# Kernel optimization log

Hardware: AMD Instinct MI355X
Metric: run time of the kernel (lower is better)

Reference implementation:

```python
import jax, jax.numpy as jnp
import numpy as np

B, Q, HID = 8, 8, 4096
H, KVH, D = 32, 8, 128
KV = 4096
ROPE_THETA = 10000.0


def rotate_half(x):
    x1, x2 = jnp.split(x, 2, axis=-1)
    return jnp.concatenate([-x2, x1], axis=-1)


def setup_inputs() -> dict:
    key = jax.random.key(0)
    ks = jax.random.split(key, 6)
    hidden_states = jax.random.normal(ks[0], (B, Q, HID), dtype=jnp.float32)
    position_ids = jnp.broadcast_to(jnp.arange(KV, dtype=jnp.int64), (B, KV))
    key_cache = jax.random.normal(ks[1], (B, KVH, KV, D), dtype=jnp.float32)
    value_cache = jax.random.normal(ks[2], (B, KVH, KV, D), dtype=jnp.float32)
    # mask: True -> blocked (-10000). Queries occupy last Q positions, causal.
    qpos = KV - Q + jnp.arange(Q)
    attention_mask = (jnp.arange(KV)[None, :] > qpos[:, None])[None, None]  # [1,1,Q,KV]
    attention_mask = jnp.broadcast_to(attention_mask, (B, 1, Q, KV))
    q_w = jax.random.normal(ks[3], (HID, HID), dtype=jnp.float32) * 0.02
    o_w = jax.random.normal(ks[4], (HID, HID), dtype=jnp.float32) * 0.02
    return {"hidden_states": hidden_states, "position_ids": position_ids,
            "key_cache": key_cache, "value_cache": value_cache,
            "attention_mask": attention_mask, "q_w": q_w, "o_w": o_w}


def reference(hidden_states, position_ids, key_cache, value_cache, attention_mask, q_w, o_w):
    # q projection: nn.Linear -> x @ W^T
    q = hidden_states @ q_w.T                       # [B,Q,HID]
    q = q.reshape(B, Q, H, D).transpose(0, 2, 1, 3)  # [B,H,Q,D]

    # rotary tables for kv_seq_len positions
    half = D // 2
    inv_freq = 1.0 / (ROPE_THETA ** (jnp.arange(0, half, dtype=jnp.float32) / half))
    t = jnp.arange(KV, dtype=jnp.float32)
    freqs = t[:, None] * inv_freq[None, :]           # [KV, D/2]
    emb = jnp.concatenate([freqs, freqs], axis=-1)   # [KV, D]
    cos_t, sin_t = jnp.cos(emb), jnp.sin(emb)

    # position_idx trick from the module: single effective rope position
    idx = jnp.argmax(position_ids.astype(jnp.int32), axis=1)[0]
    pid = jnp.take(position_ids, idx[None], axis=1)  # [B,1]
    cos = cos_t[pid][:, None]                        # [B,1,1,D]
    sin = sin_t[pid][:, None]
    q = q * cos + rotate_half(q) * sin               # [B,H,Q,D]

    # GQA attention without materializing repeat_kv (same math)
    G = H // KVH
    qg = q.reshape(B, KVH, G, Q, D)
    scores = jnp.einsum('bkgqd,bksd->bkgqs', qg, key_cache) / jnp.sqrt(jnp.float32(D))
    mask = attention_mask[:, :, None]                # [B,1,1,Q,KV]
    scores = jnp.where(mask, jnp.float32(-10000.0), scores)
    probs = jax.nn.softmax(scores.astype(jnp.float32), axis=-1).astype(q.dtype)
    out = jnp.einsum('bkgqs,bksd->bkgqd', probs, value_cache)  # [B,KVH,G,Q,D]
    out = out.reshape(B, H, Q, D).transpose(0, 2, 1, 3).reshape(B, Q, HID)
    return out @ o_w.T
```

## Files before the change

kernel.cpp:

```cpp
#include <hip/hip_runtime.h>
#include <math.h>

#define B_   8
#define Q_   8
#define HID  4096
#define NH   32
#define KVH_ 8
#define GQ   4
#define D_   128
#define KV_  4096
#define M_   64

#define OFF_COS   0
#define OFF_SIN   512
#define OFF_QROPE 1024
#define OFF_ATT   (OFF_QROPE + M_*HID)
#define OFF_OPART (OFF_ATT + M_*HID)
#define OFF_MPART (OFF_OPART + 64*8*32*128)
#define OFF_LPART (OFF_MPART + 64*8*32)
#define OFF_GPART (OFF_LPART + 64*8*32)

__global__ void prep_kernel(const int* __restrict__ pos, float* __restrict__ ws) {
    __shared__ int sv[256], si[256];
    __shared__ int s_idx;
    int t = threadIdx.x;
    int bv = -2147483647 - 1, bi = 0x7fffffff;
    for (int i = t; i < KV_; i += 256) {
        int v = pos[i];
        if (v > bv || (v == bv && i < bi)) { bv = v; bi = i; }
    }
    sv[t] = bv; si[t] = bi;
    __syncthreads();
    for (int off = 128; off > 0; off >>= 1) {
        if (t < off) {
            int v2 = sv[t + off], i2 = si[t + off];
            if (v2 > sv[t] || (v2 == sv[t] && i2 < si[t])) { sv[t] = v2; si[t] = i2; }
        }
        __syncthreads();
    }
    if (t == 0) s_idx = si[0];
    __syncthreads();
    int idx = s_idx;
    for (int u = t; u < B_ * 64; u += 256) {
        int b = u >> 6, d = u & 63;
        int pid = pos[b * KV_ + idx];
        float inv = __expf(-(float)d * (9.210340371976184f / 64.0f));
        float f = (float)pid * inv;
        ws[OFF_COS + u] = cosf(f);
        ws[OFF_SIN + u] = sinf(f);
    }
}

__global__ __launch_bounds__(128) void gemm_part(const float* __restrict__ A,
                                                 const float* __restrict__ W,
                                                 float* __restrict__ part) {
    __shared__ __align__(16) float As[32][68];
    __shared__ __align__(16) float Ws[32][132];
    int nc = blockIdx.x, kc = blockIdx.y;
    int t = threadIdx.x;
    int k0 = kc * 256;
    int n0 = nc * 128;
    int tx = t & 15, ty = t >> 4;
    float acc[2][2][4][4];
    #pragma unroll
    for (int a = 0; a < 2; a++)
        for (int bq = 0; bq < 2; bq++)
            for (int i = 0; i < 4; i++)
                for (int j = 0; j < 4; j++) acc[a][bq][i][j] = 0.f;

    for (int kt = 0; kt < 8; ++kt) {
        int kb = k0 + kt * 32;
        __syncthreads();
        {
            int m = t & 63, qh = t >> 6;
            #pragma unroll
            for (int c = 0; c < 4; ++c) {
                int q = qh * 4 + c;
                float4 v = *(const float4*)(A + (size_t)m * HID + kb + q * 4);
                As[q*4+0][m] = v.x; As[q*4+1][m] = v.y; As[q*4+2][m] = v.z; As[q*4+3][m] = v.w;
            }
        }
        {
            int n = t;
            const float* wr = W + (size_t)(n0 + n) * HID + kb;
            #pragma unroll
            for (int c = 0; c < 8; ++c) {
                float4 v = *(const float4*)(wr + c * 4);
                Ws[c*4+0][n] = v.x; Ws[c*4+1][n] = v.y; Ws[c*4+2][n] = v.z; Ws[c*4+3][n] = v.w;
            }
        }
        __syncthreads();
        #pragma unroll
        for (int kk = 0; kk < 32; ++kk) {
            float4 a0 = *(const float4*)&As[kk][ty * 4];
            float4 a1 = *(const float4*)&As[kk][32 + ty * 4];
            float4 w0 = *(const float4*)&Ws[kk][tx * 4];
            float4 w1 = *(const float4*)&Ws[kk][64 + tx * 4];
            float am[2][4] = {{a0.x,a0.y,a0.z,a0.w},{a1.x,a1.y,a1.z,a1.w}};
            float wn[2][4] = {{w0.x,w0.y,w0.z,w0.w},{w1.x,w1.y,w1.z,w1.w}};
            #pragma unroll
            for (int a = 0; a < 2; a++)
            #pragma unroll
            for (int bq = 0; bq < 2; bq++)
            #pragma unroll
            for (int i = 0; i < 4; i++)
            #pragma unroll
            for (int j = 0; j < 4; j++)
                acc[a][bq][i][j] += am[a][i] * wn[bq][j];
        }
    }
    #pragma unroll
    for (int a = 0; a < 2; a++) {
        #pragma unroll
        for (int i = 0; i < 4; i++) {
            int m = a * 32 + ty * 4 + i;
            float* dst = part + ((size_t)kc * 64 + m) * HID + n0;
            #pragma unroll
            for (int bq = 0; bq < 2; bq++) {
                float4 v;
                v.x = acc[a][bq][i][0]; v.y = acc[a][bq][i][1];
                v.z = acc[a][bq][i][2]; v.w = acc[a][bq][i][3];
                *(float4*)(dst + bq * 64 + tx * 4) = v;
            }
        }
    }
}

__global__ void qrope_kernel(float* ws) {
    const float* part = ws + OFF_GPART;
    int blk = blockIdx.x;
    int b = blk >> 5, h = blk & 31;
    int t = threadIdx.x;
    int qq = t >> 5, dl = t & 31;
    int m = b * 8 + qq;
    int d0 = dl * 2;
    float x0 = 0, x1 = 0, y0 = 0, y1 = 0;
    const float* pbase = part + (size_t)m * HID + h * 128;
    #pragma unroll
    for (int kc = 0; kc < 16; ++kc) {
        const float* p = pbase + (size_t)kc * 64 * HID;
        x0 += p[d0];      x1 += p[d0 + 1];
        y0 += p[d0 + 64]; y1 += p[d0 + 65];
    }
    float c0 = ws[OFF_COS + b * 64 + d0], c1 = ws[OFF_COS + b * 64 + d0 + 1];
    float s0 = ws[OFF_SIN + b * 64 + d0], s1 = ws[OFF_SIN + b * 64 + d0 + 1];
    float* qr = ws + OFF_QROPE + ((size_t)(b * 32 + h)) * Q_ * D_ + (size_t)qq * D_;
    qr[d0]      = x0 * c0 - y0 * s0;
    qr[d0 + 1]  = x1 * c1 - y1 * s1;
    qr[d0 + 64] = y0 * c0 + x0 * s0;
    qr[d0 + 65] = y1 * c1 + x1 * s1;
}

#define CHUNK 512
#define TK 64
__global__ __launch_bounds__(128) void attn_kernel(const float* __restrict__ Kc,
                                                   const float* __restrict__ Vc,
                                                   float* __restrict__ ws) {
    __shared__ __align__(16) float qT[128][36];
    __shared__ __align__(16) float kv[128 * 68];
    __shared__ __align__(16) float pT[64][36];
    __shared__ float m_st[32], l_st[32], al_st[32];

    int c = blockIdx.x, kvh = blockIdx.y, b = blockIdx.z;
    int t = threadIdx.x;
    int pair = b * 8 + kvh;
    const float* qbase = ws + OFF_QROPE + (size_t)pair * 32 * 128;
    {
        int r = t & 31, qh = t >> 5;
        #pragma unroll
        for (int cq = 0; cq < 8; ++cq) {
            int dq = qh * 8 + cq;
            float4 v = *(const float4*)(qbase + (size_t)r * 128 + dq * 4);
            qT[dq*4+0][r] = v.x; qT[dq*4+1][r] = v.y; qT[dq*4+2][r] = v.z; qT[dq*4+3][r] = v.w;
        }
    }
    if (t < 32) { m_st[t] = -INFINITY; l_st[t] = 0.f; }

    int rt = t >> 4, st = t & 15;
    int dt = t & 15;
    float o[4][8];
    #pragma unroll
    for (int i = 0; i < 4; i++)
        for (int j = 0; j < 8; j++) o[i][j] = 0.f;

    const float* Kb = Kc + ((size_t)pair * KV_ + c * CHUNK) * D_;
    const float* Vb = Vc + ((size_t)pair * KV_ + c * CHUNK) * D_;
    const float scale = 0.08838834764831845f;

    for (int T = 0; T < CHUNK / TK; ++T) {
        int s0 = T * TK;
        __syncthreads();
        {
            int s = t >> 1, half = t & 1;
            const float* kr = Kb + (size_t)(s0 + s) * D_ + half * 64;
            #pragma unroll
            for (int cq = 0; cq < 16; ++cq) {
                float4 v = *(const float4*)(kr + cq * 4);
                int d = half * 64 + cq * 4;
                kv[(d+0)*68 + s] = v.x; kv[(d+1)*68 + s] = v.y;
                kv[(d+2)*68 + s] = v.z; kv[(d+3)*68 + s] = v.w;
            }
        }
        __syncthreads();
        float S[4][4];
        #pragma unroll
        for (int i = 0; i < 4; i++)
            for (int j = 0; j < 4; j++) S[i][j] = 0.f;
        #pragma unroll 4
        for (int d = 0; d < 128; ++d) {
            float4 q4 = *(const float4*)&qT[d][rt * 4];
            float4 k4 = *(const float4*)&kv[d * 68 + st * 4];
            float qa[4] = {q4.x, q4.y, q4.z, q4.w};
            float ka[4] = {k4.x, k4.y, k4.z, k4.w};
            #pragma unroll
            for (int i = 0; i < 4; i++)
            #pragma unroll
            for (int j = 0; j < 4; j++)
                S[i][j] += qa[i] * ka[j];
        }
        int sabs_base = c * CHUNK + s0 + st * 4;
        #pragma unroll
        for (int i = 0; i < 4; i++) {
            int r = rt * 4 + i;
            int qq = r & 7;
            int qpos = KV_ - Q_ + qq;
            float v[4];
            float rmax = -INFINITY;
            #pragma unroll
            for (int j = 0; j < 4; j++) {
                int sa = sabs_base + j;
                float x = (sa > qpos) ? -10000.0f : S[i][j] * scale;
                v[j] = x;
                rmax = fmaxf(rmax, x);
            }
            for (int ml = 1; ml <= 8; ml <<= 1) rmax = fmaxf(rmax, __shfl_xor(rmax, ml, 64));
            float m_old = m_st[r];
            float m_new = fmaxf(m_old, rmax);
            float al = __expf(m_old - m_new);
            float ps = 0.f;
            #pragma unroll
            for (int j = 0; j < 4; j++) {
                float p = __expf(v[j] - m_new);
                pT[st * 4 + j][r] = p;
                ps += p;
            }
            for (int ml = 1; ml <= 8; ml <<= 1) ps += __shfl_xor(ps, ml, 64);
            if (st == 0) {
                l_st[r] = l_st[r] * al + ps;
                m_st[r] = m_new;
                al_st[r] = al;
            }
        }
        __syncthreads();
        {
            int s = t >> 1, half = t & 1;
            const float* vr = Vb + (size_t)(s0 + s) * D_ + half * 64;
            float* dst = &kv[s * 132 + half * 64];
            #pragma unroll
            for (int cq = 0; cq < 16; ++cq)
                *(float4*)(dst + cq * 4) = *(const float4*)(vr + cq * 4);
        }
        __syncthreads();
        float al4[4];
        #pragma unroll
        for (int i = 0; i < 4; i++) al4[i] = al_st[rt * 4 + i];
        #pragma unroll
        for (int i = 0; i < 4; i++)
            for (int j = 0; j < 8; j++) o[i][j] *= al4[i];
        #pragma unroll 2
        for (int s = 0; s < TK; ++s) {
            float4 p4 = *(const float4*)&pT[s][rt * 4];
            float4 v0 = *(const float4*)&kv[s * 132 + dt * 8];
            float4 v1 = *(const float4*)&kv[s * 132 + dt * 8 + 4];
            float pp[4] = {p4.x, p4.y, p4.z, p4.w};
            float vv[8] = {v0.x, v0.y, v0.z, v0.w, v1.x, v1.y, v1.z, v1.w};
            #pragma unroll
            for (int i = 0; i < 4; i++)
            #pragma unroll
            for (int j = 0; j < 8; j++)
                o[i][j] += pp[i] * vv[j];
        }
    }
    float* opart = ws + OFF_OPART + ((size_t)pair * 8 + c) * 32 * 128;
    #pragma unroll
    for (int i = 0; i < 4; i++) {
        int r = rt * 4 + i;
        float* dst = opart + (size_t)r * 128 + dt * 8;
        float4 v0, v1;
        v0.x = o[i][0]; v0.y = o[i][1]; v0.z = o[i][2]; v0.w = o[i][3];
        v1.x = o[i][4]; v1.y = o[i][5]; v1.z = o[i][6]; v1.w = o[i][7];
        *(float4*)dst = v0; *(float4*)(dst + 4) = v1;
    }
    __syncthreads();
    if (t < 32) {
        ws[OFF_MPART + ((size_t)pair * 8 + c) * 32 + t] = m_st[t];
        ws[OFF_LPART + ((size_t)pair * 8 + c) * 32 + t] = l_st[t];
    }
}

__global__ void combine_kernel(float* ws) {
    __shared__ float w_sh[8][32];
    int pair = blockIdx.x;
    int b = pair >> 3, kvh = pair & 7;
    int t = threadIdx.x;
    if (t < 32) {
        int r = t;
        float M = -INFINITY;
        float mv[8];
        #pragma unroll
        for (int cc = 0; cc < 8; ++cc) {
            mv[cc] = ws[OFF_MPART + ((size_t)pair * 8 + cc) * 32 + r];
            M = fmaxf(M, mv[cc]);
        }
        float L = 0.f;
        float e[8];
        #pragma unroll
        for (int cc = 0; cc < 8; ++cc) {
            e[cc] = __expf(mv[cc] - M);
            L += e[cc] * ws[OFF_LPART + ((size_t)pair * 8 + cc) * 32 + r];
        }
        float invL = 1.f / L;
        #pragma unroll
        for (int cc = 0; cc < 8; ++cc) w_sh[cc][r] = e[cc] * invL;
    }
    __syncthreads();
    const float* opart = ws + OFF_OPART + (size_t)pair * 8 * 32 * 128;
    float* aout = ws + OFF_ATT;
    for (int idx = t; idx < 32 * 128; idx += 256) {
        int r = idx >> 7, d = idx & 127;
        float acc = 0.f;
        #pragma unroll
        for (int cc = 0; cc < 8; ++cc)
            acc += w_sh[cc][r] * opart[((size_t)cc * 32 + r) * 128 + d];
        int g = r >> 3, qq = r & 7;
        aout[((size_t)(b * 8 + qq)) * HID + (kvh * 4 + g) * 128 + d] = acc;
    }
}

__global__ void oreduce_kernel(const float* __restrict__ part, float* __restrict__ out) {
    int idx = blockIdx.x * 256 + threadIdx.x;
    float4 acc = {0, 0, 0, 0};
    const float4* p = (const float4*)part;
    #pragma unroll
    for (int kc = 0; kc < 16; ++kc) {
        float4 v = p[(size_t)kc * 65536 + idx];
        acc.x += v.x; acc.y += v.y; acc.z += v.z; acc.w += v.w;
    }
    ((float4*)out)[idx] = acc;
}

extern "C" void kernel_launch(void* const* d_in, const int* in_sizes, int n_in,
                              void* d_out, int out_size, void* d_ws, size_t ws_size,
                              hipStream_t stream) {
    const float* hidden = (const float*)d_in[0];
    const int*   pos    = (const int*)d_in[1];
    const float* kcache = (const float*)d_in[2];
    const float* vcache = (const float*)d_in[3];
    const float* qw = (const float*)d_in[5];
    const float* ow = (const float*)d_in[6];
    float* ws  = (float*)d_ws;
    float* out = (float*)d_out;
    float* gpart = ws + OFF_GPART;

    prep_kernel<<<1, 256, 0, stream>>>(pos, ws);
    gemm_part<<<dim3(32, 16), 128, 0, stream>>>(hidden, qw, gpart);
    qrope_kernel<<<256, 256, 0, stream>>>(ws);
    attn_kernel<<<dim3(8, 8, 8), 128, 0, stream>>>(kcache, vcache, ws);
    combine_kernel<<<64, 256, 0, stream>>>(ws);
    gemm_part<<<dim3(32, 16), 128, 0, stream>>>(ws + OFF_ATT, ow, gpart);
    oreduce_kernel<<<256, 256, 0, stream>>>(gpart, out);
}
```

Before: 500.0 us.

## Double-buffer GEMM tiles, halve N tile, split attention over 256 threads

The GEMM now uses 64-wide N tiles, which doubles the grid to 1024 blocks, and double-buffers its shared-memory tiles with register prefetch of the next K slice, so there is one barrier per step. The attention kernel moves to 256 threads: QK^T is split across two D halves and combined with a lane shuffle, and the PV product reads V directly from global memory instead of staging it in shared memory, which removes a barrier pair. The aim is more parallelism, latency hiding, and less shared-memory traffic. The cost is more blocks and possibly uncoalesced or repeated global V reads.

```diff
diff --git a/kernel.cpp b/kernel.cpp
--- a/kernel.cpp
+++ b/kernel.cpp
@@ -54,75 +54,80 @@
 __global__ __launch_bounds__(128) void gemm_part(const float* __restrict__ A,
                                                  const float* __restrict__ W,
                                                  float* __restrict__ part) {
-    __shared__ __align__(16) float As[32][68];
-    __shared__ __align__(16) float Ws[32][132];
+    __shared__ __align__(16) float As[2][32][68];
+    __shared__ __align__(16) float Ws[2][32][68];
     int nc = blockIdx.x, kc = blockIdx.y;
     int t = threadIdx.x;
     int k0 = kc * 256;
-    int n0 = nc * 128;
+    int n0 = nc * 64;
     int tx = t & 15, ty = t >> 4;
-    float acc[2][2][4][4];
-    #pragma unroll
-    for (int a = 0; a < 2; a++)
-        for (int bq = 0; bq < 2; bq++)
-            for (int i = 0; i < 4; i++)
-                for (int j = 0; j < 4; j++) acc[a][bq][i][j] = 0.f;
-
+    int sr = t & 63, sq = t >> 6;
+
+    const float* arow = A + (size_t)sr * HID + k0 + sq * 16;
+    const float* wrow = W + (size_t)(n0 + sr) * HID + k0 + sq * 16;
+
+    float acc[8][4];
+    #pragma unroll
+    for (int i = 0; i < 8; i++)
+        #pragma unroll
+        for (int j = 0; j < 4; j++) acc[i][j] = 0.f;
+
+    #pragma unroll
+    for (int c = 0; c < 4; ++c) {
+        float4 av = *(const float4*)(arow + c * 4);
+        float4 wv = *(const float4*)(wrow + c * 4);
+        int q = sq * 4 + c;
+        As[0][q*4+0][sr] = av.x; As[0][q*4+1][sr] = av.y;
+        As[0][q*4+2][sr] = av.z; As[0][q*4+3][sr] = av.w;
+        Ws[0][q*4+0][sr] = wv.x; Ws[0][q*4+1][sr] = wv.y;
+        Ws[0][q*4+2][sr] = wv.z; Ws[0][q*4+3][sr] = wv.w;
+    }
+    __syncthreads();
+
+    int cur = 0;
     for (int kt = 0; kt < 8; ++kt) {
-        int kb = k0 + kt * 32;
-        __syncthreads();
-        {
-            int m = t & 63, qh = t >> 6;
+        float4 ra[4], rw[4];
+        if (kt < 7) {
             #pragma unroll
             for (int c = 0; c < 4; ++c) {
-                int q = qh * 4 + c;
-                float4 v = *(const float4*)(A + (size_t)m * HID + kb + q * 4);
-                As[q*4+0][m] = v.x; As[q*4+1][m] = v.y; As[q*4+2][m] = v.z; As[q*4+3][m] = v.w;
-            }
-        }
-        {
-            int n = t;
-            const float* wr = W + (size_t)(n0 + n) * HID + kb;
-            #pragma unroll
-            for (int c = 0; c < 8; ++c) {
-                float4 v = *(const float4*)(wr + c * 4);
-                Ws[c*4+0][n] = v.x; Ws[c*4+1][n] = v.y; Ws[c*4+2][n] = v.z; Ws[c*4+3][n] = v.w;
-            }
-        }
-        __syncthreads();
+                ra[c] = *(const float4*)(arow + (kt + 1) * 32 + c * 4);
+                rw[c] = *(const float4*)(wrow + (kt + 1) * 32 + c * 4);
+            }
+        }
         #pragma unroll
         for (int kk = 0; kk < 32; ++kk) {
-            float4 a0 = *(const float4*)&As[kk][ty * 4];
-            float4 a1 = *(const float4*)&As[kk][32 + ty * 4];
-            float4 w0 = *(const float4*)&Ws[kk][tx * 4];
-            float4 w1 = *(const float4*)&Ws[kk][64 + tx * 4];
-            float am[2][4] = {{a0.x,a0.y,a0.z,a0.w},{a1.x,a1.y,a1.z,a1.w}};
-            float wn[2][4] = {{w0.x,w0.y,w0.z,w0.w},{w1.x,w1.y,w1.z,w1.w}};
-            #pragma unroll
-            for (int a = 0; a < 2; a++)
-            #pragma unroll
-            for (int bq = 0; bq < 2; bq++)
-            #pragma unroll
-            for (int i = 0; i < 4; i++)
-            #pragma unroll
-            for (int j = 0; j < 4; j++)
-                acc[a][bq][i][j] += am[a][i] * wn[bq][j];
-        }
-    }
-    #pragma unroll
-    for (int a = 0; a < 2; a++) {
-        #pragma unroll
-        for (int i = 0; i < 4; i++) {
-            int m = a * 32 + ty * 4 + i;
-            float* dst = part + ((size_t)kc * 64 + m) * HID + n0;
-            #pragma unroll
-            for (int bq = 0; bq < 2; bq++) {
-                float4 v;
-                v.x = acc[a][bq][i][0]; v.y = acc[a][bq][i][1];
-                v.z = acc[a][bq][i][2]; v.w = acc[a][bq][i][3];
-                *(float4*)(dst + bq * 64 + tx * 4) = v;
-            }
-        }
+            float4 a0 = *(const float4*)&As[cur][kk][ty * 8];
+            float4 a1 = *(const float4*)&As[cur][kk][ty * 8 + 4];
+            float4 w0 = *(const float4*)&Ws[cur][kk][tx * 4];
+            float am[8] = {a0.x,a0.y,a0.z,a0.w,a1.x,a1.y,a1.z,a1.w};
+            float wn[4] = {w0.x,w0.y,w0.z,w0.w};
+            #pragma unroll
+            for (int i = 0; i < 8; i++)
+                #pragma unroll
+                for (int j = 0; j < 4; j++)
+                    acc[i][j] += am[i] * wn[j];
+        }
+        if (kt < 7) {
+            int nb = cur ^ 1;
+            #pragma unroll
+            for (int c = 0; c < 4; ++c) {
+                int q = sq * 4 + c;
+                As[nb][q*4+0][sr] = ra[c].x; As[nb][q*4+1][sr] = ra[c].y;
+                As[nb][q*4+2][sr] = ra[c].z; As[nb][q*4+3][sr] = ra[c].w;
+                Ws[nb][q*4+0][sr] = rw[c].x; Ws[nb][q*4+1][sr] = rw[c].y;
+                Ws[nb][q*4+2][sr] = rw[c].z; Ws[nb][q*4+3][sr] = rw[c].w;
+            }
+            __syncthreads();
+            cur = nb;
+        }
+    }
+    #pragma unroll
+    for (int i = 0; i < 8; i++) {
+        int m = ty * 8 + i;
+        float* dst = part + ((size_t)kc * 64 + m) * HID + n0 + tx * 4;
+        float4 v;
+        v.x = acc[i][0]; v.y = acc[i][1]; v.z = acc[i][2]; v.w = acc[i][3];
+        *(float4*)dst = v;
     }
 }
 
@@ -153,11 +158,11 @@
 
 #define CHUNK 512
 #define TK 64
-__global__ __launch_bounds__(128) void attn_kernel(const float* __restrict__ Kc,
+__global__ __launch_bounds__(256) void attn_kernel(const float* __restrict__ Kc,
                                                    const float* __restrict__ Vc,
                                                    float* __restrict__ ws) {
     __shared__ __align__(16) float qT[128][36];
-    __shared__ __align__(16) float kv[128 * 68];
+    __shared__ __align__(16) float kT[128][68];
     __shared__ __align__(16) float pT[64][36];
     __shared__ float m_st[32], l_st[32], al_st[32];
 
@@ -168,20 +173,25 @@
     {
         int r = t & 31, qh = t >> 5;
         #pragma unroll
-        for (int cq = 0; cq < 8; ++cq) {
-            int dq = qh * 8 + cq;
+        for (int cq = 0; cq < 4; ++cq) {
+            int dq = qh + cq * 8;
             float4 v = *(const float4*)(qbase + (size_t)r * 128 + dq * 4);
-            qT[dq*4+0][r] = v.x; qT[dq*4+1][r] = v.y; qT[dq*4+2][r] = v.z; qT[dq*4+3][r] = v.w;
+            qT[dq*4+0][r] = v.x; qT[dq*4+1][r] = v.y;
+            qT[dq*4+2][r] = v.z; qT[dq*4+3][r] = v.w;
         }
     }
     if (t < 32) { m_st[t] = -INFINITY; l_st[t] = 0.f; }
 
-    int rt = t >> 4, st = t & 15;
-    int dt = t & 15;
-    float o[4][8];
+    int st = t & 15;
+    int dh = (t >> 4) & 1;
+    int rt = t >> 5;
+    int dt = t & 31;
+
+    float o[4][4];
     #pragma unroll
     for (int i = 0; i < 4; i++)
-        for (int j = 0; j < 8; j++) o[i][j] = 0.f;
+        #pragma unroll
+        for (int j = 0; j < 4; j++) o[i][j] = 0.f;
 
     const float* Kb = Kc + ((size_t)pair * KV_ + c * CHUNK) * D_;
     const float* Vb = Vc + ((size_t)pair * KV_ + c * CHUNK) * D_;
@@ -191,25 +201,28 @@
         int s0 = T * TK;
         __syncthreads();
         {
-            int s = t >> 1, half = t & 1;
-            const float* kr = Kb + (size_t)(s0 + s) * D_ + half * 64;
-            #pragma unroll
-            for (int cq = 0; cq < 16; ++cq) {
-                float4 v = *(const float4*)(kr + cq * 4);
-                int d = half * 64 + cq * 4;
-                kv[(d+0)*68 + s] = v.x; kv[(d+1)*68 + s] = v.y;
-                kv[(d+2)*68 + s] = v.z; kv[(d+3)*68 + s] = v.w;
+            int s = t >> 2, qr = t & 3;
+            const float* kr = Kb + (size_t)(s0 + s) * D_ + qr * 4;
+            #pragma unroll
+            for (int cq = 0; cq < 8; ++cq) {
+                float4 v = *(const float4*)(kr + cq * 16);
+                int d = qr * 4 + cq * 16;
+                kT[d+0][s] = v.x; kT[d+1][s] = v.y;
+                kT[d+2][s] = v.z; kT[d+3][s] = v.w;
             }
         }
         __syncthreads();
         float S[4][4];
         #pragma unroll
         for (int i = 0; i < 4; i++)
+            #pragma unroll
             for (int j = 0; j < 4; j++) S[i][j] = 0.f;
+        int dbase = dh * 64;
         #pragma unroll 4
-        for (int d = 0; d < 128; ++d) {
+        for (int dd = 0; dd < 64; ++dd) {
+            int d = dbase + dd;
             float4 q4 = *(const float4*)&qT[d][rt * 4];
-            float4 k4 = *(const float4*)&kv[d * 68 + st * 4];
+            float4 k4 = *(const float4*)&kT[d][st * 4];
             float qa[4] = {q4.x, q4.y, q4.z, q4.w};
             float ka[4] = {k4.x, k4.y, k4.z, k4.w};
             #pragma unroll
@@ -218,6 +231,11 @@
             for (int j = 0; j < 4; j++)
                 S[i][j] += qa[i] * ka[j];
         }
+        #pragma unroll
+        for (int i = 0; i < 4; i++)
+            #pragma unroll
+            for (int j = 0; j < 4; j++)
+                S[i][j] += __shfl_xor(S[i][j], 16, 64);
         int sabs_base = c * CHUNK + s0 + st * 4;
         #pragma unroll
         for (int i = 0; i < 4; i++) {
@@ -241,43 +259,35 @@
             #pragma unroll
             for (int j = 0; j < 4; j++) {
                 float p = __expf(v[j] - m_new);
-                pT[st * 4 + j][r] = p;
+                if (dh == 0) pT[st * 4 + j][r] = p;
                 ps += p;
             }
             for (int ml = 1; ml <= 8; ml <<= 1) ps += __shfl_xor(ps, ml, 64);
-            if (st == 0) {
+            if (st == 0 && dh == 0) {
                 l_st[r] = l_st[r] * al + ps;
                 m_st[r] = m_new;
                 al_st[r] = al;
             }
         }
         __syncthreads();
-        {
-            int s = t >> 1, half = t & 1;
-            const float* vr = Vb + (size_t)(s0 + s) * D_ + half * 64;
-            float* dst = &kv[s * 132 + half * 64];
-            #pragma unroll
-            for (int cq = 0; cq < 16; ++cq)
-                *(float4*)(dst + cq * 4) = *(const float4*)(vr + cq * 4);
-        }
-        __syncthreads();
         float al4[4];
         #pragma unroll
         for (int i = 0; i < 4; i++) al4[i] = al_st[rt * 4 + i];
         #pragma unroll
         for (int i = 0; i < 4; i++)
-            for (int j = 0; j < 8; j++) o[i][j] *= al4[i];
-        #pragma unroll 2
+            #pragma unroll
+            for (int j = 0; j < 4; j++) o[i][j] *= al4[i];
+        const float* Vg = Vb + (size_t)s0 * D_ + dt * 4;
+        #pragma unroll 8
         for (int s = 0; s < TK; ++s) {
             float4 p4 = *(const float4*)&pT[s][rt * 4];
-            float4 v0 = *(const float4*)&kv[s * 132 + dt * 8];
-            float4 v1 = *(const float4*)&kv[s * 132 + dt * 8 + 4];
+            float4 v4 = *(const float4*)(Vg + (size_t)s * D_);
             float pp[4] = {p4.x, p4.y, p4.z, p4.w};
-            float vv[8] = {v0.x, v0.y, v0.z, v0.w, v1.x, v1.y, v1.z, v1.w};
+            float vv[4] = {v4.x, v4.y, v4.z, v4.w};
             #pragma unroll
             for (int i = 0; i < 4; i++)
             #pragma unroll
-            for (int j = 0; j < 8; j++)
+            for (int j = 0; j < 4; j++)
                 o[i][j] += pp[i] * vv[j];
         }
     }
@@ -285,11 +295,10 @@
     #pragma unroll
     for (int i = 0; i < 4; i++) {
         int r = rt * 4 + i;
-        float* dst = opart + (size_t)r * 128 + dt * 8;
-        float4 v0, v1;
-        v0.x = o[i][0]; v0.y = o[i][1]; v0.z = o[i][2]; v0.w = o[i][3];
-        v1.x = o[i][4]; v1.y = o[i][5]; v1.z = o[i][6]; v1.w = o[i][7];
-        *(float4*)dst = v0; *(float4*)(dst + 4) = v1;
+        float* dst = opart + (size_t)r * 128 + dt * 4;
+        float4 v;
+        v.x = o[i][0]; v.y = o[i][1]; v.z = o[i][2]; v.w = o[i][3];
+        *(float4*)dst = v;
     }
     __syncthreads();
     if (t < 32) {
@@ -363,10 +372,10 @@
     float* gpart = ws + OFF_GPART;
 
     prep_kernel<<<1, 256, 0, stream>>>(pos, ws);
-    gemm_part<<<dim3(32, 16), 128, 0, stream>>>(hidden, qw, gpart);
+    gemm_part<<<dim3(64, 16), 128, 0, stream>>>(hidden, qw, gpart);
     qrope_kernel<<<256, 256, 0, stream>>>(ws);
-    attn_kernel<<<dim3(8, 8, 8), 128, 0, stream>>>(kcache, vcache, ws);
+    attn_kernel<<<dim3(8, 8, 8), 256, 0, stream>>>(kcache, vcache, ws);
     combine_kernel<<<64, 256, 0, stream>>>(ws);
-    gemm_part<<<dim3(32, 16), 128, 0, stream>>>(ws + OFF_ATT, ow, gpart);
+    gemm_part<<<dim3(64, 16), 128, 0, stream>>>(ws + OFF_ATT, ow, gpart);
     oreduce_kernel<<<256, 256, 0, stream>>>(gpart, out);
 }
```

Result: faster. 489.7 us (-2.0%).
